# Kernel optimization log

Measured on AMD Instinct MI355X. Metric: run time of the kernel, lower is better.

## Reference

```python
import jax, jax.numpy as jnp
import numpy as np

DG = 8   # deformable_groups
KK = 9   # 3x3 kernel
NEG_SLOPE = 0.2


def conv3x3(x, w, b):
    y = jax.lax.conv_general_dilated(x, w, (1, 1), ((1, 1), (1, 1)),
                                     dimension_numbers=('NCHW', 'OIHW', 'NCHW'))
    return y + b[None, :, None, None]


def deform_sample(x, oy, ox, mask):
    # x: [B,C,H,W]; oy/ox/mask: [B,DG,KK,H,W] -> sampled [B,DG,cpg,KK,H,W]
    B, C, H, W = x.shape
    cpg = C // DG
    ky, kx = jnp.meshgrid(jnp.arange(3), jnp.arange(3), indexing='ij')
    ky = (ky.reshape(-1) - 1).astype(x.dtype)  # dilation=1, padding=1
    kx = (kx.reshape(-1) - 1).astype(x.dtype)
    hh = jnp.arange(H, dtype=x.dtype)
    ww = jnp.arange(W, dtype=x.dtype)
    py = hh[None, None, None, :, None] + ky[None, None, :, None, None] + oy
    px = ww[None, None, None, None, :] + kx[None, None, :, None, None] + ox
    y0 = jnp.floor(py)
    x0 = jnp.floor(px)
    fy = py - y0
    fx = px - x0
    xg = x.reshape(B, DG, cpg, H * W)

    def gather(yi, xi):
        valid = ((yi >= 0) & (yi < H) & (xi >= 0) & (xi < W)).astype(x.dtype)
        yc = jnp.clip(yi, 0, H - 1)
        xc = jnp.clip(xi, 0, W - 1)
        idx = (yc * W + xc).reshape(B, DG, 1, KK * H * W)
        v = jnp.take_along_axis(xg, idx, axis=3).reshape(B, DG, cpg, KK, H, W)
        return v * valid[:, :, None]

    y0i = y0.astype(jnp.int32)
    x0i = x0.astype(jnp.int32)
    v00 = gather(y0i, x0i)
    v01 = gather(y0i, x0i + 1)
    v10 = gather(y0i + 1, x0i)
    v11 = gather(y0i + 1, x0i + 1)
    wy = fy[:, :, None]
    wx = fx[:, :, None]
    val = (v00 * (1 - wy) * (1 - wx) + v01 * (1 - wy) * wx
           + v10 * wy * (1 - wx) + v11 * wy * wx)
    return val * mask[:, :, None]


def reference(x, offset, w_off, b_off, w_dcn, b_dcn, w_conv1, b_conv1):
    B, C, H, W = x.shape
    om = conv3x3(offset, w_off, b_off)  # [B, 3*DG*KK, H, W]
    o1, o2, m = jnp.split(om, 3, axis=1)
    oy = o1.reshape(B, DG, KK, H, W)
    ox = o2.reshape(B, DG, KK, H, W)
    mask = jax.nn.sigmoid(m).reshape(B, DG, KK, H, W)
    sampled = deform_sample(x, oy, ox, mask)  # [B,DG,cpg,KK,H,W]
    wd = w_dcn.reshape(w_dcn.shape[0], DG, C // DG, KK)
    dcn = jnp.einsum('bgckhw,ogck->bohw', sampled, wd) + b_dcn[None, :, None, None]
    fea = jnp.where(dcn >= 0, dcn, NEG_SLOPE * dcn)  # LeakyReLU(0.2)
    out = conv3x3(fea, w_conv1, b_conv1) + x  # residual
    return out


def setup_inputs() -> dict:
    key = jax.random.key(0)
    ks = jax.random.split(key, 8)
    B, C, H, W = 4, 64, 96, 96
    offC = 64
    s = 1.0 / np.sqrt(C * 9)
    return {
        'x': jax.random.normal(ks[0], (B, C, H, W), jnp.float32),
        'offset': jax.random.normal(ks[1], (B, offC, H, W), jnp.float32),
        'w_off': jax.random.normal(ks[2], (3 * DG * KK, offC, 3, 3), jnp.float32) * 0.05,
        'b_off': jnp.zeros((3 * DG * KK,), jnp.float32),
        'w_dcn': jax.random.normal(ks[3], (C, C, 3, 3), jnp.float32) * s,
        'b_dcn': jnp.zeros((C,), jnp.float32),
        'w_conv1': jax.random.normal(ks[4], (C, C, 3, 3), jnp.float32) * s,
        'b_conv1': jnp.zeros((C,), jnp.float32),
    }
```

## Files before the change

kernel.cpp:

```cpp
#include <hip/hip_runtime.h>
#include <math.h>

#define HH 96
#define WW 96
#define NB 4
#define NC 64
#define HW (HH*WW)

typedef unsigned short u16;
typedef unsigned int   u32;
typedef __attribute__((ext_vector_type(8))) short bf16x8;
typedef __attribute__((ext_vector_type(4))) float f32x4;

__device__ inline float bf2f(u16 v) { u32 u = ((u32)v) << 16; return __uint_as_float(u); }
__device__ inline u16 f2bf(float f) {
    u32 u = __float_as_uint(f);
    return (u16)((u + 0x7FFFu + ((u >> 16) & 1u)) >> 16);
}
__device__ __forceinline__ float elemf(const u32* a, int i) {
    u32 v = a[i >> 1];
    v = (i & 1) ? (v & 0xFFFF0000u) : (v << 16);
    return __uint_as_float(v);
}

__global__ __launch_bounds__(256) void k_prep(
    const float* __restrict__ x, const float* __restrict__ offset,
    const float* __restrict__ w_off, const float* __restrict__ w_dcn,
    const float* __restrict__ w_c1,
    u16* __restrict__ xt, u16* __restrict__ ot,
    u16* __restrict__ d_off, u16* __restrict__ d_dcn, u16* __restrict__ d_c1) {
    int bx = blockIdx.x;
    int tid = threadIdx.x;
    if (bx < 288) {
        const float* src = (bx < 144) ? x : offset;
        u16* dst = (bx < 144) ? xt : ot;
        int pix = (bx % 144) * 256 + tid;
        int b = pix / HW, hw = pix % HW;
        const float* s = src + b * 64 * HW + hw;
        uint4* dp = (uint4*)(dst + pix * 64);
#pragma unroll
        for (int q = 0; q < 8; ++q) {
            u32 a0 = (u32)f2bf(s[(q*8+0)*HW]) | ((u32)f2bf(s[(q*8+1)*HW]) << 16);
            u32 a1 = (u32)f2bf(s[(q*8+2)*HW]) | ((u32)f2bf(s[(q*8+3)*HW]) << 16);
            u32 a2 = (u32)f2bf(s[(q*8+4)*HW]) | ((u32)f2bf(s[(q*8+5)*HW]) << 16);
            u32 a3 = (u32)f2bf(s[(q*8+6)*HW]) | ((u32)f2bf(s[(q*8+7)*HW]) << 16);
            dp[q] = make_uint4(a0, a1, a2, a3);
        }
        return;
    }
    int rel = bx - 288;
    int m, i0;
    if (rel < 504)      { m = 0; i0 = rel * 256; }
    else if (rel < 648) { m = 1; i0 = (rel - 504) * 256; }
    else                { m = 2; i0 = (rel - 648) * 256; }
    const float* w = (m == 0) ? w_off : ((m == 1) ? w_dcn : w_c1);
    u16* dst = (m == 0) ? d_off : ((m == 1) ? d_dcn : d_c1);
    int NT   = (m == 0) ? 14 : 4;
    int NCO  = (m == 0) ? 216 : 64;
    int i = i0 + tid;
    if (i >= 18 * NT * 512) return;
    int j = i & 7, L = (i >> 3) & 63;
    int cot = (i >> 9) % NT, t = (i >> 9) / NT;
    int k = t * 32 + ((L >> 4) << 3) + j;
    int co = cot * 16 + (L & 15);
    float v = 0.f;
    if (co < NCO) {
        int ci, q;
        if (m == 1) { int c = k & 7, gk = k >> 3; int kk = gk % 9, g = gk / 9; ci = g*8+c; q = kk; }
        else        { q = k >> 6; ci = k & 63; }
        v = w[co * 576 + ci * 9 + q];
    }
    dst[i] = f2bf(v);
}

__global__ __launch_bounds__(256) void k_gemm_off(
    const u16* __restrict__ ot, const u16* __restrict__ wtb,
    const float* __restrict__ bias, u16* __restrict__ omr) {
    __shared__ u16 lb[7168];
    int tid = threadIdx.x;
    int wid = tid >> 6, L = tid & 63, lr = L & 15, lk = L >> 4;
    int pixbase = blockIdx.x * 64 + wid * 16;
    int pixA = pixbase + lr;
    int b = pixbase / HW;
    int hw = pixA % HW, y = hw / WW, x = hw % WW;

    f32x4 acc[14];
#pragma unroll
    for (int i = 0; i < 14; ++i) acc[i] = (f32x4){0.f, 0.f, 0.f, 0.f};

    for (int t = 0; t < 18; ++t) {
        if (t) __syncthreads();
        {
            const uint4* s = (const uint4*)(wtb + t * 7168);
            uint4* d = (uint4*)lb;
            for (int i = tid; i < 896; i += 256) d[i] = s[i];
        }
        __syncthreads();
        int q = t >> 1;
        int c0 = (t & 1) * 32 + lk * 8;
        int dy = q / 3 - 1, dx = q % 3 - 1;
        int yy = y + dy, xx = x + dx;
        bf16x8 a = {0,0,0,0,0,0,0,0};
        if (yy >= 0 && yy < HH && xx >= 0 && xx < WW)
            a = *(const bf16x8*)(ot + ((b * HH + yy) * WW + xx) * 64 + c0);
        const u16* wp = lb + L * 8;
#pragma unroll
        for (int cot = 0; cot < 14; ++cot) {
            bf16x8 bf = *(const bf16x8*)(wp + cot * 512);
            acc[cot] = __builtin_amdgcn_mfma_f32_16x16x32_bf16(a, bf, acc[cot], 0, 0, 0);
        }
    }
    int pixC = pixbase + lk * 4;
#pragma unroll
    for (int cot = 0; cot < 14; ++cot) {
        int co = cot * 16 + lr;
        if (co < 216) {
            int cls = co / 72;
            int c   = co % 72;
            int g   = c / 9, kk = c % 9;
            int slot = g * 32 + cls * 9 + kk;
#pragma unroll
            for (int r = 0; r < 4; ++r) {
                float v = acc[cot][r] + bias[co];
                if (cls == 2) v = 1.f / (1.f + __expf(-v));
                omr[(pixC + r) * 256 + slot] = f2bf(v);
            }
        }
    }
}

__global__ __launch_bounds__(256) void k_sdcn(
    const u16* __restrict__ xt, const u16* __restrict__ omr,
    const u16* __restrict__ wtb, const float* __restrict__ bias,
    u16* __restrict__ fea) {
    __shared__ u16 sv[32 * 576];
    int tid = threadIdx.x;
    int pixblk = blockIdx.x * 32;
    int p = tid >> 3, g = tid & 7;
    int pix = pixblk + p;
    int b = pixblk / HW;
    int hw = pix % HW, h = hw / WW, w = hw % WW;

    {
        const u16* xb = xt + b * HW * 64 + g * 8;
        const uint4* op = (const uint4*)(omr + (size_t)pix * 256 + g * 32);
        uint4 o0 = op[0], o1 = op[1], o2 = op[2], o3 = op[3];
        u32 oa[16] = {o0.x,o0.y,o0.z,o0.w, o1.x,o1.y,o1.z,o1.w,
                      o2.x,o2.y,o2.z,o2.w, o3.x,o3.y,o3.z,o3.w};
#pragma unroll
        for (int kk = 0; kk < 9; ++kk) {
            float oy   = elemf(oa, kk);
            float ox   = elemf(oa, 9 + kk);
            float mask = elemf(oa, 18 + kk);

            float py = (float)(h + kk / 3 - 1) + oy;
            float px = (float)(w + kk % 3 - 1) + ox;
            float y0f = floorf(py), x0f = floorf(px);
            float fy = py - y0f, fx = px - x0f;
            int y0 = (int)y0f, x0 = (int)x0f, y1 = y0 + 1, x1 = x0 + 1;
            int yc0 = min(max(y0, 0), HH-1), yc1 = min(max(y1, 0), HH-1);
            int xc0 = min(max(x0, 0), WW-1), xc1 = min(max(x1, 0), WW-1);
            float u0 = 1.f - fy, u1 = fy, s0 = 1.f - fx, s1 = fx;
            float w00 = (y0 >= 0 && y0 < HH && x0 >= 0 && x0 < WW) ? u0*s0*mask : 0.f;
            float w01 = (y0 >= 0 && y0 < HH && x1 >= 0 && x1 < WW) ? u0*s1*mask : 0.f;
            float w10 = (y1 >= 0 && y1 < HH && x0 >= 0 && x0 < WW) ? u1*s0*mask : 0.f;
            float w11 = (y1 >= 0 && y1 < HH && x1 >= 0 && x1 < WW) ? u1*s1*mask : 0.f;

            uint4 q00 = *(const uint4*)(xb + (yc0*WW + xc0)*64);
            uint4 q01 = *(const uint4*)(xb + (yc0*WW + xc1)*64);
            uint4 q10 = *(const uint4*)(xb + (yc1*WW + xc0)*64);
            uint4 q11 = *(const uint4*)(xb + (yc1*WW + xc1)*64);

            float r[8];
            {
                float a, bb, c, d;
                a=__uint_as_float(q00.x<<16); bb=__uint_as_float(q01.x<<16); c=__uint_as_float(q10.x<<16); d=__uint_as_float(q11.x<<16);
                r[0]=w00*a+w01*bb+w10*c+w11*d;
                a=__uint_as_float(q00.x&0xFFFF0000u); bb=__uint_as_float(q01.x&0xFFFF0000u); c=__uint_as_float(q10.x&0xFFFF0000u); d=__uint_as_float(q11.x&0xFFFF0000u);
                r[1]=w00*a+w01*bb+w10*c+w11*d;
                a=__uint_as_float(q00.y<<16); bb=__uint_as_float(q01.y<<16); c=__uint_as_float(q10.y<<16); d=__uint_as_float(q11.y<<16);
                r[2]=w00*a+w01*bb+w10*c+w11*d;
                a=__uint_as_float(q00.y&0xFFFF0000u); bb=__uint_as_float(q01.y&0xFFFF0000u); c=__uint_as_float(q10.y&0xFFFF0000u); d=__uint_as_float(q11.y&0xFFFF0000u);
                r[3]=w00*a+w01*bb+w10*c+w11*d;
                a=__uint_as_float(q00.z<<16); bb=__uint_as_float(q01.z<<16); c=__uint_as_float(q10.z<<16); d=__uint_as_float(q11.z<<16);
                r[4]=w00*a+w01*bb+w10*c+w11*d;
                a=__uint_as_float(q00.z&0xFFFF0000u); bb=__uint_as_float(q01.z&0xFFFF0000u); c=__uint_as_float(q10.z&0xFFFF0000u); d=__uint_as_float(q11.z&0xFFFF0000u);
                r[5]=w00*a+w01*bb+w10*c+w11*d;
                a=__uint_as_float(q00.w<<16); bb=__uint_as_float(q01.w<<16); c=__uint_as_float(q10.w<<16); d=__uint_as_float(q11.w<<16);
                r[6]=w00*a+w01*bb+w10*c+w11*d;
                a=__uint_as_float(q00.w&0xFFFF0000u); bb=__uint_as_float(q01.w&0xFFFF0000u); c=__uint_as_float(q10.w&0xFFFF0000u); d=__uint_as_float(q11.w&0xFFFF0000u);
                r[7]=w00*a+w01*bb+w10*c+w11*d;
            }
            u32 a0 = (u32)f2bf(r[0]) | ((u32)f2bf(r[1]) << 16);
            u32 a1 = (u32)f2bf(r[2]) | ((u32)f2bf(r[3]) << 16);
            u32 a2 = (u32)f2bf(r[4]) | ((u32)f2bf(r[5]) << 16);
            u32 a3 = (u32)f2bf(r[6]) | ((u32)f2bf(r[7]) << 16);
            int slot = g * 9 + kk;
            *(uint4*)((char*)sv + p * 1152 + ((slot * 16) ^ ((p & 7) << 4))) = make_uint4(a0, a1, a2, a3);
        }
    }
    __syncthreads();

    int wid = tid >> 6, L = tid & 63, lr = L & 15, lk = L >> 4;
    int pbase = (wid & 1) * 16, cbase = (wid >> 1) * 2;
    int arow = pbase + lr;

    f32x4 acc[2];
    acc[0] = (f32x4){0.f, 0.f, 0.f, 0.f};
    acc[1] = (f32x4){0.f, 0.f, 0.f, 0.f};
#pragma unroll
    for (int t = 0; t < 18; ++t) {
        bf16x8 a = *(const bf16x8*)((const char*)sv + arow * 1152 + (((t * 4 + lk) * 16) ^ ((arow & 7) << 4)));
#pragma unroll
        for (int ct = 0; ct < 2; ++ct) {
            bf16x8 bf = *(const bf16x8*)(wtb + ((t * 4 + cbase + ct) * 64 + L) * 8);
            acc[ct] = __builtin_amdgcn_mfma_f32_16x16x32_bf16(a, bf, acc[ct], 0, 0, 0);
        }
    }
#pragma unroll
    for (int ct = 0; ct < 2; ++ct) {
        int co = (cbase + ct) * 16 + lr;
        float bs = bias[co];
#pragma unroll
        for (int r = 0; r < 4; ++r) {
            float v = acc[ct][r] + bs;
            v = (v >= 0.f) ? v : 0.2f * v;
            fea[(pixblk + pbase + lk * 4 + r) * 64 + co] = f2bf(v);
        }
    }
}

__global__ __launch_bounds__(256) void k_gemm_c1(
    const u16* __restrict__ fea, const u16* __restrict__ wtb,
    const float* __restrict__ bias, const float* __restrict__ xres,
    float* __restrict__ out) {
    __shared__ __align__(16) char smraw[36864];
    u16* lb = (u16*)smraw;
    int tid = threadIdx.x;
    int wid = tid >> 6, L = tid & 63, lr = L & 15, lk = L >> 4;
    int pixblk = blockIdx.x * 64;
    int pixbase = pixblk + wid * 16;
    int pixA = pixbase + lr;
    int b = pixblk / HW;
    int hw = pixA % HW, y = hw / WW, x = hw % WW;

    f32x4 acc[4];
#pragma unroll
    for (int i = 0; i < 4; ++i) acc[i] = (f32x4){0.f, 0.f, 0.f, 0.f};

    {
        const uint4* s = (const uint4*)wtb;
        uint4* d = (uint4*)lb;
#pragma unroll
        for (int i = 0; i < 9; ++i) d[tid + i * 256] = s[tid + i * 256];
    }
    __syncthreads();
    for (int half = 0; half < 2; ++half) {
        int tbase = half * 9;
#pragma unroll
        for (int tl = 0; tl < 9; ++tl) {
            int t = tbase + tl;
            int q = t >> 1;
            int c0 = (t & 1) * 32 + lk * 8;
            int dy = q / 3 - 1, dx = q % 3 - 1;
            int yy = y + dy, xx = x + dx;
            bf16x8 a = {0,0,0,0,0,0,0,0};
            if (yy >= 0 && yy < HH && xx >= 0 && xx < WW)
                a = *(const bf16x8*)(fea + ((b * HH + yy) * WW + xx) * 64 + c0);
            const u16* wp = lb + (tl * 256 + L) * 8;
#pragma unroll
            for (int cot = 0; cot < 4; ++cot) {
                bf16x8 bf = *(const bf16x8*)(wp + cot * 512);
                acc[cot] = __builtin_amdgcn_mfma_f32_16x16x32_bf16(a, bf, acc[cot], 0, 0, 0);
            }
        }
        __syncthreads();
        if (half == 0) {
            const uint4* s = (const uint4*)(wtb + 18432);
            uint4* d = (uint4*)lb;
#pragma unroll
            for (int i = 0; i < 9; ++i) d[tid + i * 256] = s[tid + i * 256];
            __syncthreads();
        }
    }
    float* ob = (float*)smraw;
#pragma unroll
    for (int cot = 0; cot < 4; ++cot) {
#pragma unroll
        for (int r = 0; r < 4; ++r)
            ob[(wid * 16 + lk * 4 + r) * 66 + cot * 16 + lr] = acc[cot][r];
    }
    __syncthreads();
    int p = tid & 63, cg = tid >> 6;
    int hw0 = pixblk % HW;
#pragma unroll
    for (int i = 0; i < 16; ++i) {
        int co = cg * 16 + i;
        int idx = (b * 64 + co) * HW + hw0 + p;
        out[idx] = ob[p * 66 + co] + bias[co] + xres[idx];
    }
}

extern "C" void kernel_launch(void* const* d_in, const int* in_sizes, int n_in,
                              void* d_out, int out_size, void* d_ws, size_t ws_size,
                              hipStream_t stream) {
    const float* x       = (const float*)d_in[0];
    const float* offset  = (const float*)d_in[1];
    const float* w_off   = (const float*)d_in[2];
    const float* b_off   = (const float*)d_in[3];
    const float* w_dcn   = (const float*)d_in[4];
    const float* b_dcn   = (const float*)d_in[5];
    const float* w_conv1 = (const float*)d_in[6];
    const float* b_conv1 = (const float*)d_in[7];
    float* out = (float*)d_out;

    char* ws = (char*)d_ws;
    u16* omr     = (u16*)(ws);
    u16* xt      = (u16*)(ws + 18874368);
    u16* ot      = (u16*)(ws + 23592960);
    u16* fea     = (u16*)(ws + 28311552);
    u16* wtb_off = (u16*)(ws + 33030144);
    u16* wtb_dcn = (u16*)(ws + 33288192);
    u16* wtb_c1  = (u16*)(ws + 33361920);

    hipLaunchKernelGGL(k_prep, dim3(1080), dim3(256), 0, stream,
                       x, offset, w_off, w_dcn, w_conv1, xt, ot, wtb_off, wtb_dcn, wtb_c1);
    hipLaunchKernelGGL(k_gemm_off, dim3(576), dim3(256), 0, stream, ot, wtb_off, b_off, omr);
    hipLaunchKernelGGL(k_sdcn, dim3(1152), dim3(256), 0, stream, xt, omr, wtb_dcn, b_dcn, fea);
    hipLaunchKernelGGL(k_gemm_c1, dim3(576), dim3(256), 0, stream, fea, wtb_c1, b_conv1, x, out);
}
```

Measured before the change: 164.9 us.

## Retile offset-conv GEMM into 4x4 MFMA tiles with double-buffered weight staging

The offset conv GEMM kernel is restructured. Each wave previously covered 16 pixels across all 14 output tiles. Now each wave covers all 64 pixels of the block for 4 output-channel tiles, so each A fragment is reused across 4 MFMAs and each B fragment across 4 pixel sub-tiles. Output channels are padded to 256 (16 tiles), and the weight layout and workspace offsets change to match. Weight tiles are double-buffered in LDS with register prefetch, which drops one barrier per step. The trade-offs are wasted MFMA work on the padded channels and four times more global A loads per wave.

```diff
diff --git a/kernel.cpp b/kernel.cpp
--- a/kernel.cpp
+++ b/kernel.cpp
@@ -50,12 +50,12 @@
     }
     int rel = bx - 288;
     int m, i0;
-    if (rel < 504)      { m = 0; i0 = rel * 256; }
-    else if (rel < 648) { m = 1; i0 = (rel - 504) * 256; }
-    else                { m = 2; i0 = (rel - 648) * 256; }
+    if (rel < 576)      { m = 0; i0 = rel * 256; }
+    else if (rel < 720) { m = 1; i0 = (rel - 576) * 256; }
+    else                { m = 2; i0 = (rel - 720) * 256; }
     const float* w = (m == 0) ? w_off : ((m == 1) ? w_dcn : w_c1);
     u16* dst = (m == 0) ? d_off : ((m == 1) ? d_dcn : d_c1);
-    int NT   = (m == 0) ? 14 : 4;
+    int NT   = (m == 0) ? 16 : 4;
     int NCO  = (m == 0) ? 216 : 64;
     int i = i0 + tid;
     if (i >= 18 * NT * 512) return;
@@ -76,54 +76,85 @@
 __global__ __launch_bounds__(256) void k_gemm_off(
     const u16* __restrict__ ot, const u16* __restrict__ wtb,
     const float* __restrict__ bias, u16* __restrict__ omr) {
-    __shared__ u16 lb[7168];
+    __shared__ u16 lb[2 * 8192];
     int tid = threadIdx.x;
     int wid = tid >> 6, L = tid & 63, lr = L & 15, lk = L >> 4;
-    int pixbase = blockIdx.x * 64 + wid * 16;
-    int pixA = pixbase + lr;
-    int b = pixbase / HW;
-    int hw = pixA % HW, y = hw / WW, x = hw % WW;
-
-    f32x4 acc[14];
-#pragma unroll
-    for (int i = 0; i < 14; ++i) acc[i] = (f32x4){0.f, 0.f, 0.f, 0.f};
+    int pixblk = blockIdx.x * 64;
+    int b = pixblk / HW;
+    int yv[4], xv[4];
+#pragma unroll
+    for (int ms = 0; ms < 4; ++ms) {
+        int hw = (pixblk + ms * 16 + lr) % HW;
+        yv[ms] = hw / WW; xv[ms] = hw % WW;
+    }
+
+    f32x4 acc[4][4];
+#pragma unroll
+    for (int ms = 0; ms < 4; ++ms)
+#pragma unroll
+        for (int ct = 0; ct < 4; ++ct) acc[ms][ct] = (f32x4){0.f, 0.f, 0.f, 0.f};
+
+    uint4 rg[4];
+    {
+        const uint4* s = (const uint4*)wtb;
+#pragma unroll
+        for (int i = 0; i < 4; ++i) rg[i] = s[tid + i * 256];
+        uint4* d = (uint4*)lb;
+#pragma unroll
+        for (int i = 0; i < 4; ++i) d[tid + i * 256] = rg[i];
+    }
+    __syncthreads();
 
     for (int t = 0; t < 18; ++t) {
-        if (t) __syncthreads();
-        {
-            const uint4* s = (const uint4*)(wtb + t * 7168);
-            uint4* d = (uint4*)lb;
-            for (int i = tid; i < 896; i += 256) d[i] = s[i];
-        }
-        __syncthreads();
+        if (t + 1 < 18) {
+            const uint4* s = (const uint4*)(wtb + (t + 1) * 8192);
+#pragma unroll
+            for (int i = 0; i < 4; ++i) rg[i] = s[tid + i * 256];
+        }
         int q = t >> 1;
         int c0 = (t & 1) * 32 + lk * 8;
         int dy = q / 3 - 1, dx = q % 3 - 1;
-        int yy = y + dy, xx = x + dx;
-        bf16x8 a = {0,0,0,0,0,0,0,0};
-        if (yy >= 0 && yy < HH && xx >= 0 && xx < WW)
-            a = *(const bf16x8*)(ot + ((b * HH + yy) * WW + xx) * 64 + c0);
-        const u16* wp = lb + L * 8;
-#pragma unroll
-        for (int cot = 0; cot < 14; ++cot) {
-            bf16x8 bf = *(const bf16x8*)(wp + cot * 512);
-            acc[cot] = __builtin_amdgcn_mfma_f32_16x16x32_bf16(a, bf, acc[cot], 0, 0, 0);
-        }
-    }
-    int pixC = pixbase + lk * 4;
-#pragma unroll
-    for (int cot = 0; cot < 14; ++cot) {
-        int co = cot * 16 + lr;
-        if (co < 216) {
-            int cls = co / 72;
-            int c   = co % 72;
-            int g   = c / 9, kk = c % 9;
-            int slot = g * 32 + cls * 9 + kk;
-#pragma unroll
-            for (int r = 0; r < 4; ++r) {
-                float v = acc[cot][r] + bias[co];
-                if (cls == 2) v = 1.f / (1.f + __expf(-v));
-                omr[(pixC + r) * 256 + slot] = f2bf(v);
+        const u16* buf = lb + (t & 1) * 8192;
+        bf16x8 bfr[4];
+#pragma unroll
+        for (int ct = 0; ct < 4; ++ct)
+            bfr[ct] = *(const bf16x8*)(buf + ((wid * 4 + ct) * 64 + L) * 8);
+#pragma unroll
+        for (int ms = 0; ms < 4; ++ms) {
+            int yy = yv[ms] + dy, xx = xv[ms] + dx;
+            bf16x8 a = {0,0,0,0,0,0,0,0};
+            if (yy >= 0 && yy < HH && xx >= 0 && xx < WW)
+                a = *(const bf16x8*)(ot + ((b * HH + yy) * WW + xx) * 64 + c0);
+#pragma unroll
+            for (int ct = 0; ct < 4; ++ct)
+                acc[ms][ct] = __builtin_amdgcn_mfma_f32_16x16x32_bf16(a, bfr[ct], acc[ms][ct], 0, 0, 0);
+        }
+        if (t + 1 < 18) {
+            uint4* d = (uint4*)(lb + ((t + 1) & 1) * 8192);
+#pragma unroll
+            for (int i = 0; i < 4; ++i) d[tid + i * 256] = rg[i];
+            __syncthreads();
+        }
+    }
+
+#pragma unroll
+    for (int ms = 0; ms < 4; ++ms) {
+        int pixC = pixblk + ms * 16 + lk * 4;
+#pragma unroll
+        for (int ct = 0; ct < 4; ++ct) {
+            int co = (wid * 4 + ct) * 16 + lr;
+            if (co < 216) {
+                int cls = co / 72;
+                int c   = co % 72;
+                int g   = c / 9, kk = c % 9;
+                int slot = g * 32 + cls * 9 + kk;
+                float bs = bias[co];
+#pragma unroll
+                for (int r = 0; r < 4; ++r) {
+                    float v = acc[ms][ct][r] + bs;
+                    if (cls == 2) v = 1.f / (1.f + __expf(-v));
+                    omr[(pixC + r) * 256 + slot] = f2bf(v);
+                }
             }
         }
     }
@@ -320,10 +351,10 @@
     u16* ot      = (u16*)(ws + 23592960);
     u16* fea     = (u16*)(ws + 28311552);
     u16* wtb_off = (u16*)(ws + 33030144);
-    u16* wtb_dcn = (u16*)(ws + 33288192);
-    u16* wtb_c1  = (u16*)(ws + 33361920);
-
-    hipLaunchKernelGGL(k_prep, dim3(1080), dim3(256), 0, stream,
+    u16* wtb_dcn = (u16*)(ws + 33325056);
+    u16* wtb_c1  = (u16*)(ws + 33398784);
+
+    hipLaunchKernelGGL(k_prep, dim3(1152), dim3(256), 0, stream,
                        x, offset, w_off, w_dcn, w_conv1, xt, ot, wtb_off, wtb_dcn, wtb_c1);
     hipLaunchKernelGGL(k_gemm_off, dim3(576), dim3(256), 0, stream, ot, wtb_off, b_off, omr);
     hipLaunchKernelGGL(k_sdcn, dim3(1152), dim3(256), 0, stream, xt, omr, wtb_dcn, b_dcn, fea);
```

Result: slower. 184.0 us (+11.6%).

## Pad offset tensor with zero halo and stage offset-conv output through LDS

Applied to the files above, without the earlier changes.

The offset input is now converted into a zero-padded 98x98 NHWC bf16 buffer, so the offset-conv GEMM loads its A operand without boundary checks or branches. The offset-conv weight tile stride is padded from 14 to 16 output tiles. The scattered per-element bf16 stores of the conv output are first written into LDS and then copied to global memory with coalesced 16-byte stores. In exchange, the padded buffer takes extra workspace, the prep kernel does extra work writing the halo, and the GEMM kernel uses 32 KB of shared memory plus extra barriers.

```diff
diff --git a/kernel.cpp b/kernel.cpp
--- a/kernel.cpp
+++ b/kernel.cpp
@@ -6,6 +6,10 @@
 #define NB 4
 #define NC 64
 #define HW (HH*WW)
+#define PH 98
+#define PW 98
+#define PHW (PH*PW)
+#define NPP (NB*PHW)
 
 typedef unsigned short u16;
 typedef unsigned int   u32;
@@ -27,17 +31,15 @@
     const float* __restrict__ x, const float* __restrict__ offset,
     const float* __restrict__ w_off, const float* __restrict__ w_dcn,
     const float* __restrict__ w_c1,
-    u16* __restrict__ xt, u16* __restrict__ ot,
+    u16* __restrict__ xt, u16* __restrict__ otp,
     u16* __restrict__ d_off, u16* __restrict__ d_dcn, u16* __restrict__ d_c1) {
     int bx = blockIdx.x;
     int tid = threadIdx.x;
-    if (bx < 288) {
-        const float* src = (bx < 144) ? x : offset;
-        u16* dst = (bx < 144) ? xt : ot;
-        int pix = (bx % 144) * 256 + tid;
+    if (bx < 144) {
+        int pix = bx * 256 + tid;
         int b = pix / HW, hw = pix % HW;
-        const float* s = src + b * 64 * HW + hw;
-        uint4* dp = (uint4*)(dst + pix * 64);
+        const float* s = x + b * 64 * HW + hw;
+        uint4* dp = (uint4*)(xt + pix * 64);
 #pragma unroll
         for (int q = 0; q < 8; ++q) {
             u32 a0 = (u32)f2bf(s[(q*8+0)*HW]) | ((u32)f2bf(s[(q*8+1)*HW]) << 16);
@@ -48,14 +50,38 @@
         }
         return;
     }
-    int rel = bx - 288;
+    if (bx < 295) {
+        int pp = (bx - 144) * 256 + tid;
+        if (pp >= NPP) return;
+        int bp = pp / PHW, rem = pp % PHW;
+        int py = rem / PW, px = rem % PW;
+        int y = py - 1, xx = px - 1;
+        uint4* dp = (uint4*)(otp + (size_t)pp * 64);
+        if (y >= 0 && y < HH && xx >= 0 && xx < WW) {
+            const float* s = offset + bp * 64 * HW + y * WW + xx;
+#pragma unroll
+            for (int q = 0; q < 8; ++q) {
+                u32 a0 = (u32)f2bf(s[(q*8+0)*HW]) | ((u32)f2bf(s[(q*8+1)*HW]) << 16);
+                u32 a1 = (u32)f2bf(s[(q*8+2)*HW]) | ((u32)f2bf(s[(q*8+3)*HW]) << 16);
+                u32 a2 = (u32)f2bf(s[(q*8+4)*HW]) | ((u32)f2bf(s[(q*8+5)*HW]) << 16);
+                u32 a3 = (u32)f2bf(s[(q*8+6)*HW]) | ((u32)f2bf(s[(q*8+7)*HW]) << 16);
+                dp[q] = make_uint4(a0, a1, a2, a3);
+            }
+        } else {
+            uint4 z = make_uint4(0u, 0u, 0u, 0u);
+#pragma unroll
+            for (int q = 0; q < 8; ++q) dp[q] = z;
+        }
+        return;
+    }
+    int rel = bx - 295;
     int m, i0;
-    if (rel < 504)      { m = 0; i0 = rel * 256; }
-    else if (rel < 648) { m = 1; i0 = (rel - 504) * 256; }
-    else                { m = 2; i0 = (rel - 648) * 256; }
+    if (rel < 576)      { m = 0; i0 = rel * 256; }
+    else if (rel < 720) { m = 1; i0 = (rel - 576) * 256; }
+    else                { m = 2; i0 = (rel - 720) * 256; }
     const float* w = (m == 0) ? w_off : ((m == 1) ? w_dcn : w_c1);
     u16* dst = (m == 0) ? d_off : ((m == 1) ? d_dcn : d_c1);
-    int NT   = (m == 0) ? 14 : 4;
+    int NT   = (m == 0) ? 16 : 4;
     int NCO  = (m == 0) ? 216 : 64;
     int i = i0 + tid;
     if (i >= 18 * NT * 512) return;
@@ -74,15 +100,17 @@
 }
 
 __global__ __launch_bounds__(256) void k_gemm_off(
-    const u16* __restrict__ ot, const u16* __restrict__ wtb,
+    const u16* __restrict__ otp, const u16* __restrict__ wtb,
     const float* __restrict__ bias, u16* __restrict__ omr) {
-    __shared__ u16 lb[7168];
+    __shared__ __align__(16) char smem[32768];
+    u16* lb = (u16*)smem;
     int tid = threadIdx.x;
     int wid = tid >> 6, L = tid & 63, lr = L & 15, lk = L >> 4;
-    int pixbase = blockIdx.x * 64 + wid * 16;
-    int pixA = pixbase + lr;
-    int b = pixbase / HW;
+    int pixblk = blockIdx.x * 64;
+    int pixA = pixblk + wid * 16 + lr;
+    int b = pixblk / HW;
     int hw = pixA % HW, y = hw / WW, x = hw % WW;
+    int Abase = ((b * PH + y + 1) * PW + (x + 1)) * 64;
 
     f32x4 acc[14];
 #pragma unroll
@@ -91,18 +119,15 @@
     for (int t = 0; t < 18; ++t) {
         if (t) __syncthreads();
         {
-            const uint4* s = (const uint4*)(wtb + t * 7168);
+            const uint4* s = (const uint4*)(wtb + t * 8192);
             uint4* d = (uint4*)lb;
             for (int i = tid; i < 896; i += 256) d[i] = s[i];
         }
         __syncthreads();
         int q = t >> 1;
         int c0 = (t & 1) * 32 + lk * 8;
-        int dy = q / 3 - 1, dx = q % 3 - 1;
-        int yy = y + dy, xx = x + dx;
-        bf16x8 a = {0,0,0,0,0,0,0,0};
-        if (yy >= 0 && yy < HH && xx >= 0 && xx < WW)
-            a = *(const bf16x8*)(ot + ((b * HH + yy) * WW + xx) * 64 + c0);
+        int aoff = ((q / 3 - 1) * PW + (q % 3 - 1)) * 64 + c0;
+        bf16x8 a = *(const bf16x8*)(otp + Abase + aoff);
         const u16* wp = lb + L * 8;
 #pragma unroll
         for (int cot = 0; cot < 14; ++cot) {
@@ -110,7 +135,9 @@
             acc[cot] = __builtin_amdgcn_mfma_f32_16x16x32_bf16(a, bf, acc[cot], 0, 0, 0);
         }
     }
-    int pixC = pixbase + lk * 4;
+
+    __syncthreads();
+    u16* om_s = (u16*)smem;
 #pragma unroll
     for (int cot = 0; cot < 14; ++cot) {
         int co = cot * 16 + lr;
@@ -119,13 +146,21 @@
             int c   = co % 72;
             int g   = c / 9, kk = c % 9;
             int slot = g * 32 + cls * 9 + kk;
+            float bs = bias[co];
 #pragma unroll
             for (int r = 0; r < 4; ++r) {
-                float v = acc[cot][r] + bias[co];
+                float v = acc[cot][r] + bs;
                 if (cls == 2) v = 1.f / (1.f + __expf(-v));
-                omr[(pixC + r) * 256 + slot] = f2bf(v);
+                om_s[(wid * 16 + lk * 4 + r) * 256 + slot] = f2bf(v);
             }
         }
+    }
+    __syncthreads();
+    {
+        const uint4* s = (const uint4*)om_s;
+        uint4* d = (uint4*)(omr + (size_t)pixblk * 256);
+#pragma unroll
+        for (int i = 0; i < 8; ++i) d[tid + i * 256] = s[tid + i * 256];
     }
 }
 
@@ -317,15 +352,15 @@
     char* ws = (char*)d_ws;
     u16* omr     = (u16*)(ws);
     u16* xt      = (u16*)(ws + 18874368);
-    u16* ot      = (u16*)(ws + 23592960);
-    u16* fea     = (u16*)(ws + 28311552);
-    u16* wtb_off = (u16*)(ws + 33030144);
-    u16* wtb_dcn = (u16*)(ws + 33288192);
-    u16* wtb_c1  = (u16*)(ws + 33361920);
-
-    hipLaunchKernelGGL(k_prep, dim3(1080), dim3(256), 0, stream,
-                       x, offset, w_off, w_dcn, w_conv1, xt, ot, wtb_off, wtb_dcn, wtb_c1);
-    hipLaunchKernelGGL(k_gemm_off, dim3(576), dim3(256), 0, stream, ot, wtb_off, b_off, omr);
+    u16* otp     = (u16*)(ws + 23592960);
+    u16* fea     = (u16*)(ws + 28510208);
+    u16* wtb_off = (u16*)(ws + 33228800);
+    u16* wtb_dcn = (u16*)(ws + 33523712);
+    u16* wtb_c1  = (u16*)(ws + 33597440);
+
+    hipLaunchKernelGGL(k_prep, dim3(1159), dim3(256), 0, stream,
+                       x, offset, w_off, w_dcn, w_conv1, xt, otp, wtb_off, wtb_dcn, wtb_c1);
+    hipLaunchKernelGGL(k_gemm_off, dim3(576), dim3(256), 0, stream, otp, wtb_off, b_off, omr);
     hipLaunchKernelGGL(k_sdcn, dim3(1152), dim3(256), 0, stream, xt, omr, wtb_dcn, b_dcn, fea);
     hipLaunchKernelGGL(k_gemm_c1, dim3(576), dim3(256), 0, stream, fea, wtb_c1, b_conv1, x, out);
 }
```

New measurement: 162.0 us. About the same (-1.7%).
